# Kernel tuning notes

Measured on AMD Instinct MI355X. Metric: run time of the kernel, lower is better.

## Reference

```python
import jax, jax.numpy as jnp
import numpy as np

N0, N1, N2 = 409600, 40960, 4096   # source / mid / target node counts per sampled layer
E1, E2 = 409600, 40960             # edges in layer 1 / layer 2
F_IN, F_HID, F_OUT = 512, 256, 128


def setup_inputs() -> dict:
    key = jax.random.key(0)
    ks = jax.random.split(key, 12)
    s = 1.0 / np.sqrt(F_IN)
    s2 = 1.0 / np.sqrt(F_HID)
    return {
        "x": jax.random.normal(ks[0], (N0, F_IN), dtype=jnp.float32),
        "ei1_src": jax.random.randint(ks[1], (E1,), 0, N0),
        "ei1_dst": jax.random.randint(ks[2], (E1,), 0, N1),
        "ei2_src": jax.random.randint(ks[3], (E2,), 0, N1),
        "ei2_dst": jax.random.randint(ks[4], (E2,), 0, N2),
        "W1l": jax.random.uniform(ks[5], (F_IN, F_HID), jnp.float32, -s, s),
        "b1": jax.random.uniform(ks[6], (F_HID,), jnp.float32, -s, s),
        "W1r": jax.random.uniform(ks[7], (F_IN, F_HID), jnp.float32, -s, s),
        "W2l": jax.random.uniform(ks[8], (F_HID, F_OUT), jnp.float32, -s2, s2),
        "b2": jax.random.uniform(ks[9], (F_OUT,), jnp.float32, -s2, s2),
        "W2r": jax.random.uniform(ks[10], (F_HID, F_OUT), jnp.float32, -s2, s2),
    }


def _sage(x_src, src, dst, n_dst, Wl, b, Wr):
    # PyG SAGEConv (mean aggr): out = lin_l(mean_j x_j) + lin_r(x_target)
    msg = x_src[src]                                           # [E, F] gather
    agg = jax.ops.segment_sum(msg, dst, num_segments=n_dst)    # [n_dst, F]
    cnt = jax.ops.segment_sum(jnp.ones((src.shape[0],), x_src.dtype), dst,
                              num_segments=n_dst)
    mean = agg / jnp.maximum(cnt, 1.0)[:, None]
    x_dst = x_src[:n_dst]                                      # targets are first
    return mean @ Wl + b + x_dst @ Wr


def reference(x, ei1_src, ei1_dst, ei2_src, ei2_dst, W1l, b1, W1r, W2l, b2, W2r):
    h = _sage(x, ei1_src, ei1_dst, N1, W1l, b1, W1r)           # [N1, F_HID]
    h = jax.nn.relu(h)                                         # dropout = identity (eval)
    out = _sage(h, ei2_src, ei2_dst, N2, W2l, b2, W2r)         # [N2, F_OUT]
    return out
```

## Files before the change

### kernel.cpp

```cpp
#include <hip/hip_runtime.h>
#include <hip/hip_bf16.h>

#define N0 409600
#define N1 40960
#define N2 4096
#define E1c 409600
#define E2c 40960
#define F_IN 512
#define F_HID 256
#define F_OUT 128

using bf16x8 = __attribute__((ext_vector_type(8))) short;
using f32x4  = __attribute__((ext_vector_type(4))) float;

__device__ __forceinline__ ushort f2bf(float f) {
    union { float f; unsigned u; } v; v.f = f;
    unsigned r = v.u + 0x7fffu + ((v.u >> 16) & 1u);
    return (ushort)(r >> 16);
}
__device__ __forceinline__ float bf2f(ushort b) {
    union { unsigned u; float f; } v; v.u = ((unsigned)b) << 16;
    return v.f;
}

__device__ __forceinline__ bf16x8 load8(const ushort* p) {
    return *(const bf16x8*)p;
}
__device__ __forceinline__ bf16x8 load8(const float* p) {
    float4 a = *(const float4*)p;
    float4 b = *(const float4*)(p + 4);
    bf16x8 r;
    r[0] = (short)f2bf(a.x); r[1] = (short)f2bf(a.y);
    r[2] = (short)f2bf(a.z); r[3] = (short)f2bf(a.w);
    r[4] = (short)f2bf(b.x); r[5] = (short)f2bf(b.y);
    r[6] = (short)f2bf(b.z); r[7] = (short)f2bf(b.w);
    return r;
}

__global__ void k_hist2(const int* __restrict__ dst1, int* __restrict__ cnt1,
                        const int* __restrict__ dst2, int* __restrict__ cnt2) {
    int e = blockIdx.x * blockDim.x + threadIdx.x;
    if (e < E1c) atomicAdd(&cnt1[dst1[e]], 1);
    else {
        int e2 = e - E1c;
        if (e2 < E2c) atomicAdd(&cnt2[dst2[e2]], 1);
    }
}

__global__ __launch_bounds__(1024) void k_scanA(const int* __restrict__ cnt,
                                                int* __restrict__ off,
                                                int* __restrict__ bsum, int n) {
    __shared__ int wsum[16];
    int t = threadIdx.x, lane = t & 63, w = t >> 6;
    int i = blockIdx.x * 1024 + t;
    int v = (i < n) ? cnt[i] : 0;
    int s = v;
#pragma unroll
    for (int d = 1; d < 64; d <<= 1) {
        int u = __shfl_up(s, d, 64);
        if (lane >= d) s += u;
    }
    if (lane == 63) wsum[w] = s;
    __syncthreads();
    int wpre = 0, total = 0;
#pragma unroll
    for (int j = 0; j < 16; j++) {
        int u = wsum[j];
        if (j < w) wpre += u;
        total += u;
    }
    if (i < n) off[i] = wpre + (s - v);
    if (t == 0) bsum[blockIdx.x] = total;
}

__global__ __launch_bounds__(1024) void k_scanB(int* __restrict__ off,
                                                int* __restrict__ cursor,
                                                const int* __restrict__ bsum,
                                                int n, int nblk) {
    __shared__ int pre_s;
    int blk = blockIdx.x, t = threadIdx.x;
    if (t == 0) {
        int p = 0;
        for (int j = 0; j < blk; j++) p += bsum[j];
        pre_s = p;
        if (blk == nblk - 1) off[n] = p + bsum[blk];
    }
    __syncthreads();
    int i = blk * 1024 + t;
    if (i < n) {
        int val = off[i] + pre_s;
        off[i] = val;
        cursor[i] = val;
    }
}

__global__ void k_scatter2(const int* __restrict__ src1, const int* __restrict__ dst1,
                           int* __restrict__ cur1, int* __restrict__ perm1,
                           const int* __restrict__ src2, const int* __restrict__ dst2,
                           int* __restrict__ cur2, int* __restrict__ perm2) {
    int e = blockIdx.x * blockDim.x + threadIdx.x;
    if (e < E1c) {
        int d = dst1[e];
        int pos = atomicAdd(&cur1[d], 1);
        perm1[pos] = src1[e];
    } else {
        int e2 = e - E1c;
        if (e2 < E2c) {
            int d = dst2[e2];
            int pos = atomicAdd(&cur2[d], 1);
            perm2[pos] = src2[e2];
        }
    }
}

__global__ void k_wt_all(const float* __restrict__ W1l, const float* __restrict__ W1r,
                         const float* __restrict__ W2l, const float* __restrict__ W2r,
                         ushort* __restrict__ W1lT, ushort* __restrict__ W1rT,
                         ushort* __restrict__ W2lT, ushort* __restrict__ W2rT) {
    int idx = blockIdx.x * blockDim.x + threadIdx.x;
    const int S1 = F_IN * F_HID;
    const int S2 = F_HID * F_OUT;
    if (idx < S1) {
        int k = idx / F_HID, n = idx % F_HID;
        W1lT[(size_t)n * F_IN + k] = f2bf(W1l[idx]);
    } else if (idx < 2 * S1) {
        int j = idx - S1;
        int k = j / F_HID, n = j % F_HID;
        W1rT[(size_t)n * F_IN + k] = f2bf(W1r[j]);
    } else if (idx < 2 * S1 + S2) {
        int j = idx - 2 * S1;
        int k = j / F_OUT, n = j % F_OUT;
        W2lT[(size_t)n * F_HID + k] = f2bf(W2l[j]);
    } else if (idx < 2 * S1 + 2 * S2) {
        int j = idx - 2 * S1 - S2;
        int k = j / F_OUT, n = j % F_OUT;
        W2rT[(size_t)n * F_HID + k] = f2bf(W2r[j]);
    }
}

__global__ void k_agg1(const float* __restrict__ x, const int* __restrict__ perm,
                       const int* __restrict__ off, ushort* __restrict__ mean) {
    int d = blockIdx.x;
    int beg = off[d], end = off[d + 1];
    int t = threadIdx.x;
    const float4* xp = (const float4*)x;
    float ax = 0.f, ay = 0.f, az = 0.f, aw = 0.f;
    int e = beg;
    for (; e + 3 < end; e += 4) {
        int s0 = perm[e], s1 = perm[e + 1], s2 = perm[e + 2], s3 = perm[e + 3];
        float4 v0 = xp[(size_t)s0 * (F_IN / 4) + t];
        float4 v1 = xp[(size_t)s1 * (F_IN / 4) + t];
        float4 v2 = xp[(size_t)s2 * (F_IN / 4) + t];
        float4 v3 = xp[(size_t)s3 * (F_IN / 4) + t];
        ax += (v0.x + v1.x) + (v2.x + v3.x);
        ay += (v0.y + v1.y) + (v2.y + v3.y);
        az += (v0.z + v1.z) + (v2.z + v3.z);
        aw += (v0.w + v1.w) + (v2.w + v3.w);
    }
    for (; e < end; e++) {
        float4 v0 = xp[(size_t)perm[e] * (F_IN / 4) + t];
        ax += v0.x; ay += v0.y; az += v0.z; aw += v0.w;
    }
    int deg = end - beg;
    float inv = 1.0f / (float)(deg > 0 ? deg : 1);
    ushort4 o;
    o.x = f2bf(ax * inv); o.y = f2bf(ay * inv);
    o.z = f2bf(az * inv); o.w = f2bf(aw * inv);
    ((ushort4*)mean)[(size_t)d * (F_IN / 4) + t] = o;
}

__global__ void k_agg2(const ushort* __restrict__ h, const int* __restrict__ perm,
                       const int* __restrict__ off, ushort* __restrict__ mean) {
    int d = blockIdx.x;
    int beg = off[d], end = off[d + 1];
    int t = threadIdx.x;
    const ushort4* hp = (const ushort4*)h;
    float a0 = 0.f, a1 = 0.f, a2 = 0.f, a3 = 0.f;
    int e = beg;
    for (; e + 3 < end; e += 4) {
        ushort4 v = hp[(size_t)perm[e] * (F_HID / 4) + t];
        ushort4 u = hp[(size_t)perm[e + 1] * (F_HID / 4) + t];
        ushort4 w = hp[(size_t)perm[e + 2] * (F_HID / 4) + t];
        ushort4 z = hp[(size_t)perm[e + 3] * (F_HID / 4) + t];
        a0 += (bf2f(v.x) + bf2f(u.x)) + (bf2f(w.x) + bf2f(z.x));
        a1 += (bf2f(v.y) + bf2f(u.y)) + (bf2f(w.y) + bf2f(z.y));
        a2 += (bf2f(v.z) + bf2f(u.z)) + (bf2f(w.z) + bf2f(z.z));
        a3 += (bf2f(v.w) + bf2f(u.w)) + (bf2f(w.w) + bf2f(z.w));
    }
    for (; e < end; e++) {
        ushort4 v = hp[(size_t)perm[e] * (F_HID / 4) + t];
        a0 += bf2f(v.x); a1 += bf2f(v.y); a2 += bf2f(v.z); a3 += bf2f(v.w);
    }
    int deg = end - beg;
    float inv = 1.0f / (float)(deg > 0 ? deg : 1);
    ushort4 o;
    o.x = f2bf(a0 * inv); o.y = f2bf(a1 * inv);
    o.z = f2bf(a2 * inv); o.w = f2bf(a3 * inv);
    ((ushort4*)mean)[(size_t)d * (F_HID / 4) + t] = o;
}

#define GBK 32
#define APAD 8
template<int MF, int NF, typename TA2>
__global__ __launch_bounds__(256) void k_gemm(
    const ushort* __restrict__ A1, const TA2* __restrict__ A2,
    const ushort* __restrict__ B1T, const ushort* __restrict__ B2T,
    const float* __restrict__ bias, int M, int N, int K, int relu,
    ushort* __restrict__ Cb, float* __restrict__ Cf)
{
    constexpr int BM = 32 * MF;
    constexpr int BN = 32 * NF;
    __shared__ ushort As[BM][GBK + APAD];
    __shared__ ushort Bs[BN][GBK + APAD];
    int tid = threadIdx.x;
    int lane = tid & 63;
    int wid = tid >> 6;
    int wm = wid >> 1, wn = wid & 1;
    int bm = blockIdx.x * BM, bn = blockIdx.y * BN;

    f32x4 acc[MF][NF];
#pragma unroll
    for (int i = 0; i < MF; i++)
#pragma unroll
        for (int j = 0; j < NF; j++) acc[i][j] = (f32x4){0.f, 0.f, 0.f, 0.f};

    int sr = tid >> 2;
    int sc = (tid & 3) * 8;

    for (int part = 0; part < 2; ++part) {
        const ushort* __restrict__ B = part ? B2T : B1T;
        for (int k0 = 0; k0 < K; k0 += GBK) {
#pragma unroll
            for (int i = 0; i < BM / 64; i++) {
                int r = sr + i * 64;
                bf16x8 av = part
                    ? load8(A2 + (size_t)(bm + r) * K + k0 + sc)
                    : load8(A1 + (size_t)(bm + r) * K + k0 + sc);
                *(bf16x8*)&As[r][sc] = av;
            }
#pragma unroll
            for (int i = 0; i < BN / 64; i++) {
                int r = sr + i * 64;
                *(bf16x8*)&Bs[r][sc] = load8(B + (size_t)(bn + r) * K + k0 + sc);
            }
            __syncthreads();
            bf16x8 af[MF], bfr[NF];
            int r0 = lane & 15;
            int kq = (lane >> 4) * 8;
#pragma unroll
            for (int i = 0; i < MF; i++)
                af[i] = *(const bf16x8*)&As[wm * (MF * 16) + i * 16 + r0][kq];
#pragma unroll
            for (int j = 0; j < NF; j++)
                bfr[j] = *(const bf16x8*)&Bs[wn * (NF * 16) + j * 16 + r0][kq];
#pragma unroll
            for (int i = 0; i < MF; i++)
#pragma unroll
                for (int j = 0; j < NF; j++)
                    acc[i][j] = __builtin_amdgcn_mfma_f32_16x16x32_bf16(af[i], bfr[j], acc[i][j], 0, 0, 0);
            __syncthreads();
        }
    }

    int cn0 = lane & 15;
    int rq = (lane >> 4) * 4;
#pragma unroll
    for (int i = 0; i < MF; i++) {
#pragma unroll
        for (int j = 0; j < NF; j++) {
            int col = bn + wn * (NF * 16) + j * 16 + cn0;
            float bv = bias[col];
#pragma unroll
            for (int rr = 0; rr < 4; rr++) {
                int row = bm + wm * (MF * 16) + i * 16 + rq + rr;
                float v = acc[i][j][rr] + bv;
                if (relu) v = fmaxf(v, 0.f);
                if (Cb) Cb[(size_t)row * N + col] = f2bf(v);
                if (Cf) Cf[(size_t)row * N + col] = v;
            }
        }
    }
}

static inline size_t align256(size_t x) { return (x + 255) & ~(size_t)255; }

extern "C" void kernel_launch(void* const* d_in, const int* in_sizes, int n_in,
                              void* d_out, int out_size, void* d_ws, size_t ws_size,
                              hipStream_t stream) {
    const float* x = (const float*)d_in[0];
    const int* ei1_src = (const int*)d_in[1];
    const int* ei1_dst = (const int*)d_in[2];
    const int* ei2_src = (const int*)d_in[3];
    const int* ei2_dst = (const int*)d_in[4];
    const float* W1l = (const float*)d_in[5];
    const float* b1 = (const float*)d_in[6];
    const float* W1r = (const float*)d_in[7];
    const float* W2l = (const float*)d_in[8];
    const float* b2 = (const float*)d_in[9];
    const float* W2r = (const float*)d_in[10];
    float* out = (float*)d_out;

    char* p = (char*)d_ws;
    size_t o = 0;
    int* cnt1 = (int*)(p + o); o += (size_t)N1 * 4;
    int* cnt2 = (int*)(p + o); o = align256(o + (size_t)N2 * 4);
    int* off1 = (int*)(p + o); o = align256(o + (size_t)(N1 + 1) * 4);
    int* cur1 = (int*)(p + o); o = align256(o + (size_t)N1 * 4);
    int* perm1 = (int*)(p + o); o = align256(o + (size_t)E1c * 4);
    int* off2 = (int*)(p + o); o = align256(o + (size_t)(N2 + 1) * 4);
    int* cur2 = (int*)(p + o); o = align256(o + (size_t)N2 * 4);
    int* perm2 = (int*)(p + o); o = align256(o + (size_t)E2c * 4);
    int* bsum1 = (int*)(p + o); o = align256(o + 64 * 4);
    int* bsum2 = (int*)(p + o); o = align256(o + 64 * 4);
    ushort* mean1 = (ushort*)(p + o); o = align256(o + (size_t)N1 * F_IN * 2);
    ushort* h     = (ushort*)(p + o); o = align256(o + (size_t)N1 * F_HID * 2);
    ushort* mean2 = (ushort*)(p + o); o = align256(o + (size_t)N2 * F_HID * 2);
    ushort* W1lT  = (ushort*)(p + o); o = align256(o + (size_t)F_IN * F_HID * 2);
    ushort* W1rT  = (ushort*)(p + o); o = align256(o + (size_t)F_IN * F_HID * 2);
    ushort* W2lT  = (ushort*)(p + o); o = align256(o + (size_t)F_HID * F_OUT * 2);
    ushort* W2rT  = (ushort*)(p + o); o = align256(o + (size_t)F_HID * F_OUT * 2);

    hipMemsetAsync(cnt1, 0, (size_t)(N1 + N2) * 4, stream);

    k_hist2<<<(E1c + E2c + 255) / 256, 256, 0, stream>>>(ei1_dst, cnt1, ei2_dst, cnt2);
    k_scanA<<<N1 / 1024, 1024, 0, stream>>>(cnt1, off1, bsum1, N1);
    k_scanA<<<N2 / 1024, 1024, 0, stream>>>(cnt2, off2, bsum2, N2);
    k_scanB<<<N1 / 1024, 1024, 0, stream>>>(off1, cur1, bsum1, N1, N1 / 1024);
    k_scanB<<<N2 / 1024, 1024, 0, stream>>>(off2, cur2, bsum2, N2, N2 / 1024);
    k_scatter2<<<(E1c + E2c + 255) / 256, 256, 0, stream>>>(
        ei1_src, ei1_dst, cur1, perm1, ei2_src, ei2_dst, cur2, perm2);

    {
        int total = 2 * F_IN * F_HID + 2 * F_HID * F_OUT;
        k_wt_all<<<(total + 255) / 256, 256, 0, stream>>>(
            W1l, W1r, W2l, W2r, W1lT, W1rT, W2lT, W2rT);
    }

    k_agg1<<<N1, F_IN / 4, 0, stream>>>(x, perm1, off1, mean1);
    {
        dim3 grid(N1 / 128, F_HID / 128);
        k_gemm<4, 4, float><<<grid, 256, 0, stream>>>(mean1, x, W1lT, W1rT, b1,
                                                      N1, F_HID, F_IN, 1, h, nullptr);
    }

    k_agg2<<<N2, F_HID / 4, 0, stream>>>(h, perm2, off2, mean2);
    {
        dim3 grid(N2 / 64, F_OUT / 64);
        k_gemm<2, 2, ushort><<<grid, 256, 0, stream>>>(mean2, h, W2lT, W2rT, b2,
                                                       N2, F_OUT, F_HID, 0, nullptr, out);
    }
}
```

Measured before the change: 279.4 us.

## Fuse preprocessing kernels and retile layer-1 GEMM to full-width N blocks

Result: no change. 274.1 us (-1.9%).

```diff
diff --git a/kernel.cpp b/kernel.cpp
--- a/kernel.cpp
+++ b/kernel.cpp
@@ -37,87 +37,15 @@
     return r;
 }
 
-__global__ void k_hist2(const int* __restrict__ dst1, int* __restrict__ cnt1,
-                        const int* __restrict__ dst2, int* __restrict__ cnt2) {
-    int e = blockIdx.x * blockDim.x + threadIdx.x;
-    if (e < E1c) atomicAdd(&cnt1[dst1[e]], 1);
-    else {
-        int e2 = e - E1c;
-        if (e2 < E2c) atomicAdd(&cnt2[dst2[e2]], 1);
-    }
-}
-
-__global__ __launch_bounds__(1024) void k_scanA(const int* __restrict__ cnt,
-                                                int* __restrict__ off,
-                                                int* __restrict__ bsum, int n) {
-    __shared__ int wsum[16];
-    int t = threadIdx.x, lane = t & 63, w = t >> 6;
-    int i = blockIdx.x * 1024 + t;
-    int v = (i < n) ? cnt[i] : 0;
-    int s = v;
-#pragma unroll
-    for (int d = 1; d < 64; d <<= 1) {
-        int u = __shfl_up(s, d, 64);
-        if (lane >= d) s += u;
-    }
-    if (lane == 63) wsum[w] = s;
-    __syncthreads();
-    int wpre = 0, total = 0;
-#pragma unroll
-    for (int j = 0; j < 16; j++) {
-        int u = wsum[j];
-        if (j < w) wpre += u;
-        total += u;
-    }
-    if (i < n) off[i] = wpre + (s - v);
-    if (t == 0) bsum[blockIdx.x] = total;
-}
-
-__global__ __launch_bounds__(1024) void k_scanB(int* __restrict__ off,
-                                                int* __restrict__ cursor,
-                                                const int* __restrict__ bsum,
-                                                int n, int nblk) {
-    __shared__ int pre_s;
-    int blk = blockIdx.x, t = threadIdx.x;
-    if (t == 0) {
-        int p = 0;
-        for (int j = 0; j < blk; j++) p += bsum[j];
-        pre_s = p;
-        if (blk == nblk - 1) off[n] = p + bsum[blk];
-    }
-    __syncthreads();
-    int i = blk * 1024 + t;
-    if (i < n) {
-        int val = off[i] + pre_s;
-        off[i] = val;
-        cursor[i] = val;
-    }
-}
-
-__global__ void k_scatter2(const int* __restrict__ src1, const int* __restrict__ dst1,
-                           int* __restrict__ cur1, int* __restrict__ perm1,
-                           const int* __restrict__ src2, const int* __restrict__ dst2,
-                           int* __restrict__ cur2, int* __restrict__ perm2) {
-    int e = blockIdx.x * blockDim.x + threadIdx.x;
-    if (e < E1c) {
-        int d = dst1[e];
-        int pos = atomicAdd(&cur1[d], 1);
-        perm1[pos] = src1[e];
-    } else {
-        int e2 = e - E1c;
-        if (e2 < E2c) {
-            int d = dst2[e2];
-            int pos = atomicAdd(&cur2[d], 1);
-            perm2[pos] = src2[e2];
-        }
-    }
-}
-
-__global__ void k_wt_all(const float* __restrict__ W1l, const float* __restrict__ W1r,
-                         const float* __restrict__ W2l, const float* __restrict__ W2r,
-                         ushort* __restrict__ W1lT, ushort* __restrict__ W1rT,
-                         ushort* __restrict__ W2lT, ushort* __restrict__ W2rT) {
+__global__ void k_prep(const int* __restrict__ dst1, int* __restrict__ cnt1,
+                       const int* __restrict__ dst2, int* __restrict__ cnt2,
+                       const float* __restrict__ W1l, const float* __restrict__ W1r,
+                       const float* __restrict__ W2l, const float* __restrict__ W2r,
+                       ushort* __restrict__ W1lT, ushort* __restrict__ W1rT,
+                       ushort* __restrict__ W2lT, ushort* __restrict__ W2rT) {
     int idx = blockIdx.x * blockDim.x + threadIdx.x;
+    if (idx < E1c) atomicAdd(&cnt1[dst1[idx]], 1);
+    else if (idx - E1c < E2c) atomicAdd(&cnt2[dst2[idx - E1c]], 1);
     const int S1 = F_IN * F_HID;
     const int S2 = F_HID * F_OUT;
     if (idx < S1) {
@@ -135,6 +63,88 @@
         int j = idx - 2 * S1 - S2;
         int k = j / F_OUT, n = j % F_OUT;
         W2rT[(size_t)n * F_HID + k] = f2bf(W2r[j]);
+    }
+}
+
+#define NBLK1 (N1 / 1024)
+#define NBLK2 (N2 / 1024)
+
+__global__ __launch_bounds__(1024) void k_scanA2(const int* __restrict__ cnt1, int* __restrict__ off1,
+                                                 int* __restrict__ bsum1,
+                                                 const int* __restrict__ cnt2, int* __restrict__ off2,
+                                                 int* __restrict__ bsum2) {
+    __shared__ int wsum[16];
+    int blk = blockIdx.x;
+    const int* cnt; int* off; int* bsum; int lb;
+    if (blk < NBLK1) { cnt = cnt1; off = off1; bsum = bsum1; lb = blk; }
+    else             { cnt = cnt2; off = off2; bsum = bsum2; lb = blk - NBLK1; }
+    int t = threadIdx.x, lane = t & 63, w = t >> 6;
+    int i = lb * 1024 + t;
+    int v = cnt[i];
+    int s = v;
+#pragma unroll
+    for (int d = 1; d < 64; d <<= 1) {
+        int u = __shfl_up(s, d, 64);
+        if (lane >= d) s += u;
+    }
+    if (lane == 63) wsum[w] = s;
+    __syncthreads();
+    int wpre = 0, total = 0;
+#pragma unroll
+    for (int j = 0; j < 16; j++) {
+        int u = wsum[j];
+        if (j < w) wpre += u;
+        total += u;
+    }
+    off[i] = wpre + (s - v);
+    if (t == 0) bsum[lb] = total;
+}
+
+__global__ __launch_bounds__(1024) void k_scanB2(int* __restrict__ off1, int* __restrict__ cur1,
+                                                 const int* __restrict__ bsum1,
+                                                 int* __restrict__ off2, int* __restrict__ cur2,
+                                                 const int* __restrict__ bsum2) {
+    __shared__ int s_pre, s_tot;
+    int blk = blockIdx.x;
+    int* off; int* cur; const int* bsum; int lb, nblk, n;
+    if (blk < NBLK1) { off = off1; cur = cur1; bsum = bsum1; lb = blk;         nblk = NBLK1; n = N1; }
+    else             { off = off2; cur = cur2; bsum = bsum2; lb = blk - NBLK1; nblk = NBLK2; n = N2; }
+    int t = threadIdx.x;
+    if (t < 64) {
+        int v = (t < nblk) ? bsum[t] : 0;
+        int p = (t < lb) ? v : 0;
+        int tt = v;
+#pragma unroll
+        for (int d = 32; d >= 1; d >>= 1) {
+            p  += __shfl_xor(p, d, 64);
+            tt += __shfl_xor(tt, d, 64);
+        }
+        if (t == 0) { s_pre = p; s_tot = tt; }
+    }
+    __syncthreads();
+    int i = lb * 1024 + t;
+    int val = off[i] + s_pre;
+    off[i] = val;
+    cur[i] = val;
+    if (lb == 0 && t == 0) off[n] = s_tot;
+}
+
+__global__ void k_scatter2(const int* __restrict__ src1, const int* __restrict__ dst1,
+                           int* __restrict__ cur1, int* __restrict__ perm1,
+                           const int* __restrict__ src2, const int* __restrict__ dst2,
+                           int* __restrict__ cur2, int* __restrict__ perm2) {
+    int e = blockIdx.x * blockDim.x + threadIdx.x;
+    if (e < E1c) {
+        int d = dst1[e];
+        int pos = atomicAdd(&cur1[d], 1);
+        perm1[pos] = src1[e];
+    } else {
+        int e2 = e - E1c;
+        if (e2 < E2c) {
+            int d = dst2[e2];
+            int pos = atomicAdd(&cur2[d], 1);
+            perm2[pos] = src2[e2];
+        }
     }
 }
 
@@ -201,21 +211,22 @@
 
 #define GBK 32
 #define APAD 8
-template<int MF, int NF, typename TA2>
+template<int WM, int WN, int MF, int NF, typename TA2>
 __global__ __launch_bounds__(256) void k_gemm(
     const ushort* __restrict__ A1, const TA2* __restrict__ A2,
     const ushort* __restrict__ B1T, const ushort* __restrict__ B2T,
     const float* __restrict__ bias, int M, int N, int K, int relu,
     ushort* __restrict__ Cb, float* __restrict__ Cf)
 {
-    constexpr int BM = 32 * MF;
-    constexpr int BN = 32 * NF;
+    constexpr int BM = WM * MF * 16;
+    constexpr int BN = WN * NF * 16;
+    static_assert(BM % 64 == 0 && BN % 64 == 0, "tile must be multiple of 64");
     __shared__ ushort As[BM][GBK + APAD];
     __shared__ ushort Bs[BN][GBK + APAD];
     int tid = threadIdx.x;
     int lane = tid & 63;
     int wid = tid >> 6;
-    int wm = wid >> 1, wn = wid & 1;
+    int wm = wid / WN, wn = wid % WN;
     int bm = blockIdx.x * BM, bn = blockIdx.y * BN;
 
     f32x4 acc[MF][NF];
@@ -322,31 +333,28 @@
 
     hipMemsetAsync(cnt1, 0, (size_t)(N1 + N2) * 4, stream);
 
-    k_hist2<<<(E1c + E2c + 255) / 256, 256, 0, stream>>>(ei1_dst, cnt1, ei2_dst, cnt2);
-    k_scanA<<<N1 / 1024, 1024, 0, stream>>>(cnt1, off1, bsum1, N1);
-    k_scanA<<<N2 / 1024, 1024, 0, stream>>>(cnt2, off2, bsum2, N2);
-    k_scanB<<<N1 / 1024, 1024, 0, stream>>>(off1, cur1, bsum1, N1, N1 / 1024);
-    k_scanB<<<N2 / 1024, 1024, 0, stream>>>(off2, cur2, bsum2, N2, N2 / 1024);
+    {
+        int total = E1c + E2c;
+        k_prep<<<(total + 255) / 256, 256, 0, stream>>>(
+            ei1_dst, cnt1, ei2_dst, cnt2,
+            W1l, W1r, W2l, W2r, W1lT, W1rT, W2lT, W2rT);
+    }
+    k_scanA2<<<NBLK1 + NBLK2, 1024, 0, stream>>>(cnt1, off1, bsum1, cnt2, off2, bsum2);
+    k_scanB2<<<NBLK1 + NBLK2, 1024, 0, stream>>>(off1, cur1, bsum1, off2, cur2, bsum2);
     k_scatter2<<<(E1c + E2c + 255) / 256, 256, 0, stream>>>(
         ei1_src, ei1_dst, cur1, perm1, ei2_src, ei2_dst, cur2, perm2);
 
-    {
-        int total = 2 * F_IN * F_HID + 2 * F_HID * F_OUT;
-        k_wt_all<<<(total + 255) / 256, 256, 0, stream>>>(
-            W1l, W1r, W2l, W2r, W1lT, W1rT, W2lT, W2rT);
-    }
-
     k_agg1<<<N1, F_IN / 4, 0, stream>>>(x, perm1, off1, mean1);
     {
-        dim3 grid(N1 / 128, F_HID / 128);
-        k_gemm<4, 4, float><<<grid, 256, 0, stream>>>(mean1, x, W1lT, W1rT, b1,
-                                                      N1, F_HID, F_IN, 1, h, nullptr);
+        dim3 grid(N1 / 64, F_HID / 256);
+        k_gemm<1, 4, 4, 4, float><<<grid, 256, 0, stream>>>(mean1, x, W1lT, W1rT, b1,
+                                                            N1, F_HID, F_IN, 1, h, nullptr);
     }
 
     k_agg2<<<N2, F_HID / 4, 0, stream>>>(h, perm2, off2, mean2);
     {
         dim3 grid(N2 / 64, F_OUT / 64);
-        k_gemm<2, 2, ushort><<<grid, 256, 0, stream>>>(mean2, h, W2lT, W2rT, b2,
-                                                       N2, F_OUT, F_HID, 0, nullptr, out);
-    }
-}
+        k_gemm<2, 2, 2, 2, ushort><<<grid, 256, 0, stream>>>(mean2, h, W2lT, W2rT, b2,
+                                                             N2, F_OUT, F_HID, 0, nullptr, out);
+    }
+}
```
